# Performance work log

Measured on AMD Instinct MI355X. Metric: run time of the kernel, lower is better.

The kernel has to match this reference:

```python
import jax, jax.numpy as jnp
import numpy as np

B, S, H = 2, 1024, 4096
NH, NKV, HD = 32, 8, 128
THETA = 500000.0
EPS = 1e-6


def _ste(x, q):
    # straight-through estimator: forward q, gradient of identity
    return x + jax.lax.stop_gradient(q - x)


def weight_quant(w):
    # BitNet b1.58 ternary weight quantization (per-tensor mean-abs scale)
    scale = 1.0 / jnp.clip(jnp.mean(jnp.abs(w)), 1e-5)
    wq = jnp.clip(jnp.round(w * scale), -1.0, 1.0) / scale
    return _ste(w, wq)


def act_quant(x):
    # per-token int8 absmax activation quantization
    scale = 127.0 / jnp.clip(jnp.max(jnp.abs(x), axis=-1, keepdims=True), 1e-5)
    xq = jnp.clip(jnp.round(x * scale), -128.0, 127.0) / scale
    return _ste(x, xq)


def bitlinear(x, w):
    # torch Linear convention: w is (out, in)
    return act_quant(x) @ weight_quant(w).T


def rmsnorm(x, w):
    return x * jax.lax.rsqrt(jnp.mean(x * x, axis=-1, keepdims=True) + EPS) * w


def rope(x, cos, sin):
    # x: (b, s, h, hd); pairs are interleaved (even, odd) like view_as_complex
    x2 = x.reshape(*x.shape[:-1], HD // 2, 2)
    a, b = x2[..., 0], x2[..., 1]
    c = cos[None, :, None, :]
    s = sin[None, :, None, :]
    out = jnp.stack([a * c - b * s, a * s + b * c], axis=-1)
    return out.reshape(x.shape)


def setup_inputs() -> dict:
    key = jax.random.key(0)
    ks = jax.random.split(key, 6)
    hidden_states = jax.random.normal(ks[0], (B, S, H), dtype=jnp.float32)
    causal = jnp.tril(jnp.ones((S, S), dtype=bool))
    attention_mask = jnp.where(causal, 0.0, -1e9).astype(jnp.float32)[None, None]
    w_q = jax.random.normal(ks[1], (NH * HD, H), dtype=jnp.float32) * 0.02
    w_k = jax.random.normal(ks[2], (NKV * HD, H), dtype=jnp.float32) * 0.02
    w_v = jax.random.normal(ks[3], (NKV * HD, H), dtype=jnp.float32) * 0.02
    w_o = jax.random.normal(ks[4], (H, NH * HD), dtype=jnp.float32) * 0.02
    subln_w = jnp.ones((NH * HD,), dtype=jnp.float32)
    return {"hidden_states": hidden_states, "attention_mask": attention_mask,
            "w_q": w_q, "w_k": w_k, "w_v": w_v, "w_o": w_o, "subln_w": subln_w}


def reference(hidden_states, attention_mask, w_q, w_k, w_v, w_o, subln_w):
    b, s, _ = hidden_states.shape
    # RoPE tables (precomputed buffer in torch, constant here)
    inv_freq = 1.0 / (THETA ** (jnp.arange(0, HD, 2, dtype=jnp.float32) / HD))
    freqs = jnp.arange(s, dtype=jnp.float32)[:, None] * inv_freq[None, :]  # (s, hd/2)
    cos, sin = jnp.cos(freqs), jnp.sin(freqs)

    q = bitlinear(hidden_states, w_q).reshape(b, s, NH, HD)
    k = bitlinear(hidden_states, w_k).reshape(b, s, NKV, HD)
    v = bitlinear(hidden_states, w_v).reshape(b, s, NKV, HD)

    q = rope(q, cos, sin)
    k = rope(k, cos, sin)

    # GQA: repeat kv heads
    n_rep = NH // NKV
    k = jnp.repeat(k, n_rep, axis=2)  # (b, s, NH, hd)
    v = jnp.repeat(v, n_rep, axis=2)

    scale = 1.0 / np.sqrt(HD)
    scores = jnp.einsum('bqhd,bkhd->bhqk', q, k) * scale
    scores = scores + attention_mask
    attn = jax.nn.softmax(scores.astype(jnp.float32), axis=-1).astype(q.dtype)
    out = jnp.einsum('bhqk,bkhd->bqhd', attn, v).reshape(b, s, NH * HD)

    out = rmsnorm(out, subln_w)  # SubLN before output projection
    out = bitlinear(out, w_o)
    return out
```

## Files before the change

### kernel.cpp

```cpp
#include <hip/hip_runtime.h>
#include <hip/hip_bf16.h>
#include <cstdint>

typedef unsigned short u16;
typedef __bf16 bf16x8 __attribute__((ext_vector_type(8)));
typedef float f32x4 __attribute__((ext_vector_type(4)));
typedef int i32x4 __attribute__((ext_vector_type(4)));

#define SEQ 1024
#define HID 4096
#define NHQ 32
#define NKVH 8
#define HDIM 128
#define NB 2
#define NROWS (NB*SEQ)

static __device__ __forceinline__ u16 f2bf(float x) {
  __hip_bfloat16 h = __float2bfloat16(x);
  return *reinterpret_cast<u16*>(&h);
}

static __device__ __forceinline__ void gload16(const void* g, void* l) {
  __builtin_amdgcn_global_load_lds((__attribute__((address_space(1))) void*)(void*)g,
                                   (__attribute__((address_space(3))) void*)l, 16, 0, 0);
}

static __device__ __forceinline__ int pack4i8(float a, float b, float c, float d,
                                              float s, float lo, float hi) {
  int x0 = (int)fminf(fmaxf(rintf(a*s), lo), hi);
  int x1 = (int)fminf(fmaxf(rintf(b*s), lo), hi);
  int x2 = (int)fminf(fmaxf(rintf(c*s), lo), hi);
  int x3 = (int)fminf(fmaxf(rintf(d*s), lo), hi);
  return (x0 & 255) | ((x1 & 255) << 8) | ((x2 & 255) << 16) | ((x3 & 255) << 24);
}

__global__ __launch_bounds__(256) void k_abssum4(const float* __restrict__ wq_, const float* __restrict__ wk_,
                                                 const float* __restrict__ wv_, const float* __restrict__ wo_,
                                                 float* __restrict__ partial) {
  int bx = blockIdx.x;
  const float* w; long n4; int pbase, lb, nb;
  if (bx < 1024)      { w = wq_; n4 = 4194304; pbase = 0;    lb = bx;        nb = 1024; }
  else if (bx < 1280) { w = wk_; n4 = 1048576; pbase = 1024; lb = bx - 1024; nb = 256; }
  else if (bx < 1536) { w = wv_; n4 = 1048576; pbase = 1280; lb = bx - 1280; nb = 256; }
  else                { w = wo_; n4 = 4194304; pbase = 1536; lb = bx - 1536; nb = 1024; }
  float s = 0.f;
  long stride = (long)nb * 256;
  const float4* w4 = (const float4*)w;
  for (long j = (long)lb*256 + threadIdx.x; j < n4; j += stride) {
    float4 v = w4[j];
    s += fabsf(v.x) + fabsf(v.y) + fabsf(v.z) + fabsf(v.w);
  }
  #pragma unroll
  for (int off = 1; off < 64; off <<= 1) s += __shfl_xor(s, off);
  __shared__ float red[4];
  if ((threadIdx.x & 63) == 0) red[threadIdx.x >> 6] = s;
  __syncthreads();
  if (threadIdx.x == 0) partial[pbase + lb] = red[0] + red[1] + red[2] + red[3];
}

__global__ __launch_bounds__(256) void k_wscale(const float* __restrict__ partial,
                                                float* __restrict__ wsc) {
  __shared__ float red[4];
  const float nelem[4] = {16777216.f, 4194304.f, 4194304.f, 16777216.f};
  const int pbase[4] = {0, 1024, 1280, 1536};
  const int pcnt[4]  = {1024, 256, 256, 1024};
  for (int wi = 0; wi < 4; ++wi) {
    float s = 0.f;
    for (int j = threadIdx.x; j < pcnt[wi]; j += 256) s += partial[pbase[wi] + j];
    #pragma unroll
    for (int off = 1; off < 64; off <<= 1) s += __shfl_xor(s, off);
    if ((threadIdx.x & 63) == 0) red[threadIdx.x >> 6] = s;
    __syncthreads();
    if (threadIdx.x == 0) wsc[wi] = fmaxf((red[0]+red[1]+red[2]+red[3]) / nelem[wi], 1e-5f);
    __syncthreads();
  }
}

__global__ __launch_bounds__(256) void k_quantw8_all(const float* __restrict__ wq_, const float* __restrict__ wk_,
                                                     const float* __restrict__ wv_, const float* __restrict__ wo_,
                                                     char* __restrict__ oq_, char* __restrict__ ok_,
                                                     char* __restrict__ ov_, char* __restrict__ oo_,
                                                     const float* __restrict__ wsc) {
  int bx = blockIdx.x;
  const float* src; char* dst; int idx; long base;
  if (bx < 16384)      { src = wq_; dst = oq_; idx = 0; base = bx; }
  else if (bx < 20480) { src = wk_; dst = ok_; idx = 1; base = bx - 16384; }
  else if (bx < 24576) { src = wv_; dst = ov_; idx = 2; base = bx - 20480; }
  else                 { src = wo_; dst = oo_; idx = 3; base = bx - 24576; }
  long j = base*256 + threadIdx.x;
  long oj = j;
  if (idx <= 1) {
    long row = j >> 10;
    int u = (int)(row & 31);
    long prow = (row & ~31L) | (long)((u >> 1) | ((u & 1) << 4));
    oj = (prow << 10) | (j & 1023);
  }
  float inv = 1.0f / wsc[idx];
  float4 v = ((const float4*)src)[j];
  ((int*)dst)[oj] = pack4i8(v.x, v.y, v.z, v.w, inv, -1.f, 1.f);
}

__global__ __launch_bounds__(256) void k_actq8(const float* __restrict__ x, char* __restrict__ xq,
                                               float* __restrict__ xs) {
  long row = blockIdx.x;
  const float4* xr = (const float4*)(x + row*HID);
  float4 v[4];
  float am = 0.f;
  #pragma unroll
  for (int j = 0; j < 4; ++j) {
    v[j] = xr[j*256 + threadIdx.x];
    am = fmaxf(am, fmaxf(fmaxf(fabsf(v[j].x), fabsf(v[j].y)), fmaxf(fabsf(v[j].z), fabsf(v[j].w))));
  }
  #pragma unroll
  for (int off = 1; off < 64; off <<= 1) am = fmaxf(am, __shfl_xor(am, off));
  __shared__ float red[4];
  if ((threadIdx.x & 63) == 0) red[threadIdx.x >> 6] = am;
  __syncthreads();
  am = fmaxf(fmaxf(red[0], red[1]), fmaxf(red[2], red[3]));
  float amc = fmaxf(am, 1e-5f);
  float s = 127.0f / amc;
  int* oq = (int*)(xq + row*HID);
  #pragma unroll
  for (int j = 0; j < 4; ++j)
    oq[j*256 + threadIdx.x] = pack4i8(v[j].x, v[j].y, v[j].z, v[j].w, s, -128.f, 127.f);
  if (threadIdx.x == 0) xs[row] = amc / 127.0f;
}

__global__ __launch_bounds__(128, 2) void k_gemm8(const char* __restrict__ A, const char* __restrict__ W,
                                                  float* __restrict__ C, const float* __restrict__ arow,
                                                  const float* __restrict__ wsc, int widx,
                                                  int M, int N, int K) {
  __shared__ char As[3][128*64] __attribute__((aligned(16)));
  __shared__ char Ws_[3][128*64] __attribute__((aligned(16)));
  int t = threadIdx.x;
  int bid = blockIdx.x;
  int xcd = bid & 7, w = bid >> 3;
  int bm = ((xcd & 1) << 3) + (w >> 3);
  int bn = ((xcd >> 1) << 3) + (w & 7);
  const char* Ab = A + (long)bm*128*K;
  const char* Wb = W + (long)bn*128*K;
  int lane = t & 63, wid = t >> 6;
  int lrow = lane & 15, l8 = lane >> 4;
  int ch0 = (l8 ^ ((lrow >> 1) & 3)) * 16;
  i32x4 zero = {0, 0, 0, 0};
  i32x4 acc[4][8];
  #pragma unroll
  for (int mi = 0; mi < 4; ++mi)
    #pragma unroll
    for (int ni = 0; ni < 8; ++ni) acc[mi][ni] = zero;

  auto stage = [&](int buf, int kt) {
    #pragma unroll
    for (int i = 0; i < 4; ++i) {
      int c = t + 128*i;
      int row = c >> 2;
      int ci = ((c & 3) ^ ((row >> 1) & 3)) * 16;
      gload16(Ab + (long)row*K + kt*64 + ci, &As[buf][c*16]);
      gload16(Wb + (long)row*K + kt*64 + ci, &Ws_[buf][c*16]);
    }
  };

  int nk = K >> 6;
  stage(0, 0); stage(1, 1);
  asm volatile("s_waitcnt vmcnt(8)" ::: "memory");
  __builtin_amdgcn_sched_barrier(0);
  __builtin_amdgcn_s_barrier();
  __builtin_amdgcn_sched_barrier(0);
  for (int kt = 0; kt < nk; ++kt) {
    int cur = kt % 3;
    i32x4 af[4], bfr[8];
    #pragma unroll
    for (int mi = 0; mi < 4; ++mi) af[mi] = *(const i32x4*)&As[cur][(wid*64 + mi*16 + lrow)*64 + ch0];
    #pragma unroll
    for (int ni = 0; ni < 8; ++ni) bfr[ni] = *(const i32x4*)&Ws_[cur][(ni*16 + lrow)*64 + ch0];
    if (kt + 2 < nk) stage((kt + 2) % 3, kt + 2);
    __builtin_amdgcn_s_setprio(1);
    #pragma unroll
    for (int mi = 0; mi < 4; ++mi)
      #pragma unroll
      for (int ni = 0; ni < 8; ++ni)
        acc[mi][ni] = __builtin_amdgcn_mfma_i32_16x16x64_i8(af[mi], bfr[ni], acc[mi][ni], 0, 0, 0);
    __builtin_amdgcn_s_setprio(0);
    if (kt + 2 < nk)      asm volatile("s_waitcnt vmcnt(8)" ::: "memory");
    else if (kt + 1 < nk) asm volatile("s_waitcnt vmcnt(0)" ::: "memory");
    if (kt + 1 < nk) {
      __builtin_amdgcn_sched_barrier(0);
      __builtin_amdgcn_s_barrier();
      __builtin_amdgcn_sched_barrier(0);
    }
  }
  float ws = wsc[widx];
  #pragma unroll
  for (int mi = 0; mi < 4; ++mi)
    #pragma unroll
    for (int r = 0; r < 4; ++r) {
      int row = bm*128 + wid*64 + mi*16 + l8*4 + r;
      float sc = arow[row] * ws;
      #pragma unroll
      for (int ni = 0; ni < 8; ++ni) {
        int col = bn*128 + ni*16 + lrow;
        C[(long)row*N + col] = (float)acc[mi][ni][r] * sc;
      }
    }
}

__global__ __launch_bounds__(128, 2) void k_gemm8_qkv(const char* __restrict__ A,
    const char* __restrict__ Wq, const char* __restrict__ Wk, const char* __restrict__ Wv,
    u16* __restrict__ Qb, u16* __restrict__ Kb, u16* __restrict__ Vt,
    const float* __restrict__ arow, const float* __restrict__ wsc,
    const float* __restrict__ cosb, const float* __restrict__ sinb) {
  const int K = 4096;
  int bid = blockIdx.x;
  int xcd = bid & 7, w = bid >> 3;
  int kind, bm, bn;
  const char* W;
  if (w < 64)      { kind = 0; bm = ((xcd & 1) << 3) + (w >> 3); bn = ((xcd >> 1) << 3) + (w & 7); W = Wq; }
  else if (w < 80) { int u = w - 64; kind = 1; bm = (xcd << 1) + (u >> 3); bn = u & 7; W = Wk; }
  else             { int u = w - 80; kind = 2; bm = (xcd << 1) + (u >> 3); bn = u & 7; W = Wv; }

  __shared__ char As[3][128*64] __attribute__((aligned(16)));
  __shared__ char Ws_[3][128*64] __attribute__((aligned(16)));
  int t = threadIdx.x;
  const char* Ab = A + (long)bm*128*K;
  const char* Wb = W + (long)bn*128*K;
  int lane = t & 63, wid = t >> 6;
  int lrow = lane & 15, l8 = lane >> 4;
  int ch0 = (l8 ^ ((lrow >> 1) & 3)) * 16;
  i32x4 zero = {0, 0, 0, 0};
  i32x4 acc[4][8];
  #pragma unroll
  for (int mi = 0; mi < 4; ++mi)
    #pragma unroll
    for (int ni = 0; ni < 8; ++ni) acc[mi][ni] = zero;

  auto stage = [&](int buf, int kt) {
    #pragma unroll
    for (int i = 0; i < 4; ++i) {
      int c = t + 128*i;
      int row = c >> 2;
      int ci = ((c & 3) ^ ((row >> 1) & 3)) * 16;
      gload16(Ab + (long)row*K + kt*64 + ci, &As[buf][c*16]);
      gload16(Wb + (long)row*K + kt*64 + ci, &Ws_[buf][c*16]);
    }
  };

  int nk = K >> 6;
  stage(0, 0); stage(1, 1);
  asm volatile("s_waitcnt vmcnt(8)" ::: "memory");
  __builtin_amdgcn_sched_barrier(0);
  __builtin_amdgcn_s_barrier();
  __builtin_amdgcn_sched_barrier(0);
  for (int kt = 0; kt < nk; ++kt) {
    int cur = kt % 3;
    i32x4 af[4], bfr[8];
    #pragma unroll
    for (int mi = 0; mi < 4; ++mi) af[mi] = *(const i32x4*)&As[cur][(wid*64 + mi*16 + lrow)*64 + ch0];
    #pragma unroll
    for (int ni = 0; ni < 8; ++ni) bfr[ni] = *(const i32x4*)&Ws_[cur][(ni*16 + lrow)*64 + ch0];
    if (kt + 2 < nk) stage((kt + 2) % 3, kt + 2);
    __builtin_amdgcn_s_setprio(1);
    #pragma unroll
    for (int mi = 0; mi < 4; ++mi)
      #pragma unroll
      for (int ni = 0; ni < 8; ++ni)
        acc[mi][ni] = __builtin_amdgcn_mfma_i32_16x16x64_i8(af[mi], bfr[ni], acc[mi][ni], 0, 0, 0);
    __builtin_amdgcn_s_setprio(0);
    if (kt + 2 < nk)      asm volatile("s_waitcnt vmcnt(8)" ::: "memory");
    else if (kt + 1 < nk) asm volatile("s_waitcnt vmcnt(0)" ::: "memory");
    if (kt + 1 < nk) {
      __builtin_amdgcn_sched_barrier(0);
      __builtin_amdgcn_s_barrier();
      __builtin_amdgcn_sched_barrier(0);
    }
  }

  if (kind == 2) {
    float ws = wsc[2];
    #pragma unroll
    for (int mi = 0; mi < 4; ++mi) {
      int row0 = bm*128 + wid*64 + mi*16 + l8*4;
      int bidx = row0 >> 10, s0 = row0 & 1023;
      #pragma unroll
      for (int ni = 0; ni < 8; ++ni) {
        int col = bn*128 + ni*16 + lrow;
        int hkv = col >> 7, d = col & 127;
        ushort4 o4;
        o4.x = f2bf((float)acc[mi][ni][0] * arow[row0+0] * ws);
        o4.y = f2bf((float)acc[mi][ni][1] * arow[row0+1] * ws);
        o4.z = f2bf((float)acc[mi][ni][2] * arow[row0+2] * ws);
        o4.w = f2bf((float)acc[mi][ni][3] * arow[row0+3] * ws);
        *(ushort4*)&Vt[(((long)bidx*NKVH + hkv)*HDIM + d)*SEQ + s0] = o4;
      }
    }
  } else {
    float ws = wsc[kind];
    u16* dst = kind ? Kb : Qb;
    int nh = kind ? NKVH : NHQ;
    #pragma unroll
    for (int mi = 0; mi < 4; ++mi) {
      #pragma unroll
      for (int r = 0; r < 4; ++r) {
        int row = bm*128 + wid*64 + mi*16 + l8*4 + r;
        int bidx = row >> 10, s = row & 1023;
        float sc = arow[row] * ws;
        #pragma unroll
        for (int j = 0; j < 4; ++j) {
          float a  = (float)acc[mi][2*j][r] * sc;
          float b2 = (float)acc[mi][2*j+1][r] * sc;
          int B = bn*128 + j*32;
          int h = B >> 7;
          int d = (B & 127) + 2*lrow;
          int i = d >> 1;
          float cc = cosb[(s << 6) + i], sn = sinb[(s << 6) + i];
          ushort2 o2;
          o2.x = f2bf(a*cc - b2*sn);
          o2.y = f2bf(a*sn + b2*cc);
          *(ushort2*)&dst[(((long)bidx*nh + h)*SEQ + s)*HDIM + d] = o2;
        }
      }
    }
  }
}

__global__ __launch_bounds__(256) void k_ropetab(float* __restrict__ cosb, float* __restrict__ sinb) {
  int idx = blockIdx.x*256 + threadIdx.x;
  int s = idx >> 6, i = idx & 63;
  float e = (2.0f * (float)i) / 128.0f;
  float inv = 1.0f / powf(500000.0f, e);
  float f = (float)s * inv;
  cosb[idx] = cosf(f);
  sinb[idx] = sinf(f);
}

__global__ __launch_bounds__(256) void k_attn(const u16* __restrict__ qb, const u16* __restrict__ kb,
                                              const u16* __restrict__ vt, float* __restrict__ ao) {
  int p = blockIdx.x, h = blockIdx.y, b = blockIdx.z;
  int t = threadIdx.x, lane = t & 63, wid = t >> 6;
  int lrow = lane & 15, l8 = lane >> 4;
  int x7 = lrow & 7;

  __shared__ u16 Ks[2][64*128] __attribute__((aligned(16)));
  __shared__ u16 Vs[2][128*64] __attribute__((aligned(16)));
  __shared__ u16 Ps[4][16][72] __attribute__((aligned(16)));

  const u16* kp = kb + ((long)(b*NKVH + (h >> 2)))*SEQ*HDIM;
  const u16* vp = vt + ((long)(b*NKVH + (h >> 2)))*HDIM*SEQ;

  auto stageK = [&](int buf, int j) {
    const u16* src = kp + (long)j*64*HDIM;
    #pragma unroll
    for (int i = 0; i < 4; ++i) {
      int r0 = wid*16 + i*4;
      int row = r0 + (lane >> 4);
      int cg = (lane & 15) ^ (row & 7);
      gload16(src + (long)row*HDIM + cg*8, &Ks[buf][r0*HDIM]);
    }
  };
  auto stageV = [&](int buf, int j) {
    #pragma unroll
    for (int i = 0; i < 4; ++i) {
      int r0 = wid*32 + i*8;
      int row = r0 + (lane >> 3);
      int cg = (lane & 7) ^ (row & 7);
      gload16(vp + (long)row*SEQ + j*64 + cg*8, &Vs[buf][r0*64]);
    }
  };

  for (int phase = 0; phase < 2; ++phase) {
    int qt = phase ? (15 - p) : p;
    int q0 = qt*64 + wid*16;
    const u16* qp = qb + (((long)(b*NHQ + h))*SEQ + q0)*HDIM;
    bf16x8 qf[4];
    #pragma unroll
    for (int ks = 0; ks < 4; ++ks) qf[ks] = *(const bf16x8*)&qp[lrow*HDIM + ks*32 + l8*8];
    f32x4 zero = {0.f, 0.f, 0.f, 0.f};
    f32x4 o[8];
    #pragma unroll
    for (int f = 0; f < 8; ++f) o[f] = zero;
    float m[4], ll[4];
    #pragma unroll
    for (int r = 0; r < 4; ++r) { m[r] = -1e30f; ll[r] = 0.f; }

    int nj = qt + 1;
    stageK(0, 0); stageV(0, 0);
    __syncthreads();
    int cur = 0;
    for (int j = 0; j < nj; ++j) {
      if (j + 1 < nj) { stageK(cur ^ 1, j + 1); stageV(cur ^ 1, j + 1); }
      const u16* Kc = Ks[cur];
      const u16* Vc = Vs[cur];
      f32x4 sc4[4];
      #pragma unroll
      for (int ni = 0; ni < 4; ++ni) sc4[ni] = zero;
      __builtin_amdgcn_s_setprio(1);
      #pragma unroll
      for (int ni = 0; ni < 4; ++ni) {
        int row = ni*16 + lrow;
        #pragma unroll
        for (int ks = 0; ks < 4; ++ks) {
          int cl = (ks*4 + l8) ^ x7;
          bf16x8 kfr = *(const bf16x8*)&Kc[row*HDIM + cl*8];
          sc4[ni] = __builtin_amdgcn_mfma_f32_16x16x32_bf16(qf[ks], kfr, sc4[ni], 0, 0, 0);
        }
      }
      __builtin_amdgcn_s_setprio(0);
      const float scale = 0.08838834764831845f;
      float pm[4] = {-1e30f, -1e30f, -1e30f, -1e30f};
      float pv[4][4];
      bool diag = (j == qt);
      #pragma unroll
      for (int ni = 0; ni < 4; ++ni) {
        int kv = j*64 + ni*16 + lrow;
        #pragma unroll
        for (int r = 0; r < 4; ++r) {
          int qr = q0 + l8*4 + r;
          float val = sc4[ni][r] * scale;
          if (diag && kv > qr) val = -1e30f;
          pv[ni][r] = val;
          pm[r] = fmaxf(pm[r], val);
        }
      }
      #pragma unroll
      for (int r = 0; r < 4; ++r) {
        #pragma unroll
        for (int off = 1; off < 16; off <<= 1) pm[r] = fmaxf(pm[r], __shfl_xor(pm[r], off));
      }
      float fr[4], rs[4];
      #pragma unroll
      for (int r = 0; r < 4; ++r) {
        float nm = fmaxf(m[r], pm[r]);
        fr[r] = __expf(m[r] - nm);
        m[r] = nm; rs[r] = 0.f;
      }
      #pragma unroll
      for (int ni = 0; ni < 4; ++ni)
        #pragma unroll
        for (int r = 0; r < 4; ++r) {
          float pe = __expf(pv[ni][r] - m[r]);
          pv[ni][r] = pe; rs[r] += pe;
        }
      #pragma unroll
      for (int r = 0; r < 4; ++r) {
        #pragma unroll
        for (int off = 1; off < 16; off <<= 1) rs[r] += __shfl_xor(rs[r], off);
        ll[r] = ll[r]*fr[r] + rs[r];
      }
      #pragma unroll
      for (int f = 0; f < 8; ++f) {
        o[f][0] *= fr[0]; o[f][1] *= fr[1]; o[f][2] *= fr[2]; o[f][3] *= fr[3];
      }
      #pragma unroll
      for (int ni = 0; ni < 4; ++ni)
        #pragma unroll
        for (int r = 0; r < 4; ++r)
          Ps[wid][l8*4 + r][ni*16 + lrow] = f2bf(pv[ni][r]);
      bf16x8 pf0 = *(const bf16x8*)&Ps[wid][lrow][l8*8];
      bf16x8 pf1 = *(const bf16x8*)&Ps[wid][lrow][32 + l8*8];
      __builtin_amdgcn_s_setprio(1);
      #pragma unroll
      for (int f = 0; f < 8; ++f) {
        int d = f*16 + lrow;
        bf16x8 v0 = *(const bf16x8*)&Vc[d*64 + ((l8) ^ x7)*8];
        bf16x8 v1 = *(const bf16x8*)&Vc[d*64 + ((4 + l8) ^ x7)*8];
        o[f] = __builtin_amdgcn_mfma_f32_16x16x32_bf16(pf0, v0, o[f], 0, 0, 0);
        o[f] = __builtin_amdgcn_mfma_f32_16x16x32_bf16(pf1, v1, o[f], 0, 0, 0);
      }
      __builtin_amdgcn_s_setprio(0);
      __syncthreads();
      cur ^= 1;
    }
    float invl[4];
    #pragma unroll
    for (int r = 0; r < 4; ++r) invl[r] = 1.0f / ll[r];
    #pragma unroll
    for (int f = 0; f < 8; ++f)
      #pragma unroll
      for (int r = 0; r < 4; ++r) {
        long row = (long)b*SEQ + q0 + l8*4 + r;
        ao[row*HID + h*HDIM + f*16 + lrow] = o[f][r] * invl[r];
      }
    __syncthreads();
  }
}

__global__ __launch_bounds__(256) void k_rmsq8(const float* __restrict__ x, const float* __restrict__ w,
                                               char* __restrict__ yq, float* __restrict__ ys) {
  long row = blockIdx.x;
  const float4* xr = (const float4*)(x + row*HID);
  const float4* wr = (const float4*)w;
  float4 v[4];
  float ss = 0.f;
  #pragma unroll
  for (int j = 0; j < 4; ++j) {
    v[j] = xr[j*256 + threadIdx.x];
    ss += v[j].x*v[j].x + v[j].y*v[j].y + v[j].z*v[j].z + v[j].w*v[j].w;
  }
  #pragma unroll
  for (int off = 1; off < 64; off <<= 1) ss += __shfl_xor(ss, off);
  __shared__ float red[4];
  if ((threadIdx.x & 63) == 0) red[threadIdx.x >> 6] = ss;
  __syncthreads();
  ss = red[0] + red[1] + red[2] + red[3];
  __syncthreads();
  float rn = rsqrtf(ss / (float)HID + 1e-6f);
  float4 y[4];
  float am = 0.f;
  #pragma unroll
  for (int j = 0; j < 4; ++j) {
    float4 wv = wr[j*256 + threadIdx.x];
    y[j].x = v[j].x * rn * wv.x; y[j].y = v[j].y * rn * wv.y;
    y[j].z = v[j].z * rn * wv.z; y[j].w = v[j].w * rn * wv.w;
    am = fmaxf(am, fmaxf(fmaxf(fabsf(y[j].x), fabsf(y[j].y)), fmaxf(fabsf(y[j].z), fabsf(y[j].w))));
  }
  #pragma unroll
  for (int off = 1; off < 64; off <<= 1) am = fmaxf(am, __shfl_xor(am, off));
  if ((threadIdx.x & 63) == 0) red[threadIdx.x >> 6] = am;
  __syncthreads();
  am = fmaxf(fmaxf(red[0], red[1]), fmaxf(red[2], red[3]));
  float amc = fmaxf(am, 1e-5f);
  float s = 127.0f / amc;
  int* oq = (int*)(yq + row*HID);
  #pragma unroll
  for (int j = 0; j < 4; ++j)
    oq[j*256 + threadIdx.x] = pack4i8(y[j].x, y[j].y, y[j].z, y[j].w, s, -128.f, 127.f);
  if (threadIdx.x == 0) ys[row] = amc / 127.0f;
}

extern "C" void kernel_launch(void* const* d_in, const int* in_sizes, int n_in,
                              void* d_out, int out_size, void* d_ws, size_t ws_size,
                              hipStream_t stream) {
  const float* hs    = (const float*)d_in[0];
  const float* w_q   = (const float*)d_in[2];
  const float* w_k   = (const float*)d_in[3];
  const float* w_v   = (const float*)d_in[4];
  const float* w_o   = (const float*)d_in[5];
  const float* subln = (const float*)d_in[6];

  char* ws = (char*)d_ws;
  char*  wqq = (char*)(ws + 0L);
  char*  wqk = (char*)(ws + 16777216L);
  char*  wqv = (char*)(ws + 20971520L);
  char*  wqo = (char*)(ws + 25165824L);
  char*  xq  = (char*)(ws + 41943040L);
  float* ao  = (float*)(ws + 50331648L);
  char*  yq  = (char*)(ws + 83886080L);
  u16*   qb  = (u16*)(ws + 92274688L);
  u16*   kb  = (u16*)(ws + 109051904L);
  u16*   vtb = (u16*)(ws + 113246208L);
  float* cosb= (float*)(ws + 117440512L);
  float* sinb= (float*)(ws + 117702656L);
  float* xs  = (float*)(ws + 117964800L);
  float* ys  = (float*)(ws + 117972992L);
  float* wsc = (float*)(ws + 117981184L);
  float* par = (float*)(ws + 117981248L);
  float* out = (float*)d_out;

  k_abssum4<<<2560, 256, 0, stream>>>(w_q, w_k, w_v, w_o, par);
  k_wscale<<<1, 256, 0, stream>>>(par, wsc);

  k_quantw8_all<<<40960, 256, 0, stream>>>(w_q, w_k, w_v, w_o, wqq, wqk, wqv, wqo, wsc);
  k_ropetab<<<256, 256, 0, stream>>>(cosb, sinb);
  k_actq8<<<NROWS, 256, 0, stream>>>(hs, xq, xs);

  k_gemm8_qkv<<<768, 128, 0, stream>>>(xq, wqq, wqk, wqv, qb, kb, vtb, xs, wsc, cosb, sinb);

  k_attn<<<dim3(8, 32, 2), 256, 0, stream>>>(qb, kb, vtb, ao);

  k_rmsq8<<<NROWS, 256, 0, stream>>>(ao, subln, yq, ys);

  k_gemm8<<<512, 128, 0, stream>>>(yq, wqo, out, ys, wsc, 3, NROWS, 4096, 4096);
}
```

Before: 245.9 us.

## Load A operand directly into registers, bypassing LDS in int8 GEMMs

In both int8 GEMM kernels, each wave now loads its own A-operand rows straight from global memory into registers. A one-step register double buffer (afC/afN) holds the fragments, and the k-loop is unrolled by two so the buffers swap each step. A is no longer staged through LDS, and only W keeps the triple-buffered LDS path. This drops A's LDS writes and reads and halves shared memory use, since A rows are private to each wave. The explicit vmcnt waits are removed, so visibility of the LDS-DMA loads for W now depends on the compiler's in-order waits on the A register loads. The k-loop also now assumes an even tile count.

Result: slower. 278.3 us (+13.2%).

```diff
diff --git a/kernel.cpp b/kernel.cpp
--- a/kernel.cpp
+++ b/kernel.cpp
@@ -130,7 +130,6 @@
                                                   float* __restrict__ C, const float* __restrict__ arow,
                                                   const float* __restrict__ wsc, int widx,
                                                   int M, int N, int K) {
-  __shared__ char As[3][128*64] __attribute__((aligned(16)));
   __shared__ char Ws_[3][128*64] __attribute__((aligned(16)));
   int t = threadIdx.x;
   int bid = blockIdx.x;
@@ -142,6 +141,7 @@
   int lane = t & 63, wid = t >> 6;
   int lrow = lane & 15, l8 = lane >> 4;
   int ch0 = (l8 ^ ((lrow >> 1) & 3)) * 16;
+  const char* Aw = Ab + (long)(wid*64 + lrow)*K + l8*16;
   i32x4 zero = {0, 0, 0, 0};
   i32x4 acc[4][8];
   #pragma unroll
@@ -155,40 +155,49 @@
       int c = t + 128*i;
       int row = c >> 2;
       int ci = ((c & 3) ^ ((row >> 1) & 3)) * 16;
-      gload16(Ab + (long)row*K + kt*64 + ci, &As[buf][c*16]);
       gload16(Wb + (long)row*K + kt*64 + ci, &Ws_[buf][c*16]);
     }
   };
+  auto loadA = [&](i32x4* dst, int kt) {
+    #pragma unroll
+    for (int mi = 0; mi < 4; ++mi)
+      dst[mi] = *(const i32x4*)(Aw + (long)mi*16*K + kt*64);
+  };
 
   int nk = K >> 6;
+  i32x4 afC[4], afN[4];
   stage(0, 0); stage(1, 1);
+  loadA(afC, 0);
   asm volatile("s_waitcnt vmcnt(8)" ::: "memory");
   __builtin_amdgcn_sched_barrier(0);
   __builtin_amdgcn_s_barrier();
   __builtin_amdgcn_sched_barrier(0);
-  for (int kt = 0; kt < nk; ++kt) {
-    int cur = kt % 3;
-    i32x4 af[4], bfr[8];
-    #pragma unroll
-    for (int mi = 0; mi < 4; ++mi) af[mi] = *(const i32x4*)&As[cur][(wid*64 + mi*16 + lrow)*64 + ch0];
-    #pragma unroll
-    for (int ni = 0; ni < 8; ++ni) bfr[ni] = *(const i32x4*)&Ws_[cur][(ni*16 + lrow)*64 + ch0];
+
+  auto body = [&](int kt, i32x4* cur, i32x4* nxt) {
+    int cb = kt % 3;
+    i32x4 bfr[8];
+    #pragma unroll
+    for (int ni = 0; ni < 8; ++ni) bfr[ni] = *(const i32x4*)&Ws_[cb][(ni*16 + lrow)*64 + ch0];
     if (kt + 2 < nk) stage((kt + 2) % 3, kt + 2);
+    if (kt + 1 < nk) loadA(nxt, kt + 1);
     __builtin_amdgcn_s_setprio(1);
     #pragma unroll
     for (int mi = 0; mi < 4; ++mi)
       #pragma unroll
       for (int ni = 0; ni < 8; ++ni)
-        acc[mi][ni] = __builtin_amdgcn_mfma_i32_16x16x64_i8(af[mi], bfr[ni], acc[mi][ni], 0, 0, 0);
+        acc[mi][ni] = __builtin_amdgcn_mfma_i32_16x16x64_i8(cur[mi], bfr[ni], acc[mi][ni], 0, 0, 0);
     __builtin_amdgcn_s_setprio(0);
-    if (kt + 2 < nk)      asm volatile("s_waitcnt vmcnt(8)" ::: "memory");
-    else if (kt + 1 < nk) asm volatile("s_waitcnt vmcnt(0)" ::: "memory");
     if (kt + 1 < nk) {
       __builtin_amdgcn_sched_barrier(0);
       __builtin_amdgcn_s_barrier();
       __builtin_amdgcn_sched_barrier(0);
     }
-  }
+  };
+  for (int k2 = 0; k2 < nk; k2 += 2) {
+    body(k2, afC, afN);
+    body(k2 + 1, afN, afC);
+  }
+
   float ws = wsc[widx];
   #pragma unroll
   for (int mi = 0; mi < 4; ++mi)
@@ -218,7 +227,6 @@
   else if (w < 80) { int u = w - 64; kind = 1; bm = (xcd << 1) + (u >> 3); bn = u & 7; W = Wk; }
   else             { int u = w - 80; kind = 2; bm = (xcd << 1) + (u >> 3); bn = u & 7; W = Wv; }
 
-  __shared__ char As[3][128*64] __attribute__((aligned(16)));
   __shared__ char Ws_[3][128*64] __attribute__((aligned(16)));
   int t = threadIdx.x;
   const char* Ab = A + (long)bm*128*K;
@@ -226,6 +234,7 @@
   int lane = t & 63, wid = t >> 6;
   int lrow = lane & 15, l8 = lane >> 4;
   int ch0 = (l8 ^ ((lrow >> 1) & 3)) * 16;
+  const char* Aw = Ab + (long)(wid*64 + lrow)*K + l8*16;
   i32x4 zero = {0, 0, 0, 0};
   i32x4 acc[4][8];
   #pragma unroll
@@ -239,39 +248,47 @@
       int c = t + 128*i;
       int row = c >> 2;
       int ci = ((c & 3) ^ ((row >> 1) & 3)) * 16;
-      gload16(Ab + (long)row*K + kt*64 + ci, &As[buf][c*16]);
       gload16(Wb + (long)row*K + kt*64 + ci, &Ws_[buf][c*16]);
     }
   };
+  auto loadA = [&](i32x4* dst, int kt) {
+    #pragma unroll
+    for (int mi = 0; mi < 4; ++mi)
+      dst[mi] = *(const i32x4*)(Aw + (long)mi*16*K + kt*64);
+  };
 
   int nk = K >> 6;
+  i32x4 afC[4], afN[4];
   stage(0, 0); stage(1, 1);
+  loadA(afC, 0);
   asm volatile("s_waitcnt vmcnt(8)" ::: "memory");
   __builtin_amdgcn_sched_barrier(0);
   __builtin_amdgcn_s_barrier();
   __builtin_amdgcn_sched_barrier(0);
-  for (int kt = 0; kt < nk; ++kt) {
-    int cur = kt % 3;
-    i32x4 af[4], bfr[8];
-    #pragma unroll
-    for (int mi = 0; mi < 4; ++mi) af[mi] = *(const i32x4*)&As[cur][(wid*64 + mi*16 + lrow)*64 + ch0];
-    #pragma unroll
-    for (int ni = 0; ni < 8; ++ni) bfr[ni] = *(const i32x4*)&Ws_[cur][(ni*16 + lrow)*64 + ch0];
+
+  auto body = [&](int kt, i32x4* cur, i32x4* nxt) {
+    int cb = kt % 3;
+    i32x4 bfr[8];
+    #pragma unroll
+    for (int ni = 0; ni < 8; ++ni) bfr[ni] = *(const i32x4*)&Ws_[cb][(ni*16 + lrow)*64 + ch0];
     if (kt + 2 < nk) stage((kt + 2) % 3, kt + 2);
+    if (kt + 1 < nk) loadA(nxt, kt + 1);
     __builtin_amdgcn_s_setprio(1);
     #pragma unroll
     for (int mi = 0; mi < 4; ++mi)
       #pragma unroll
       for (int ni = 0; ni < 8; ++ni)
-        acc[mi][ni] = __builtin_amdgcn_mfma_i32_16x16x64_i8(af[mi], bfr[ni], acc[mi][ni], 0, 0, 0);
+        acc[mi][ni] = __builtin_amdgcn_mfma_i32_16x16x64_i8(cur[mi], bfr[ni], acc[mi][ni], 0, 0, 0);
     __builtin_amdgcn_s_setprio(0);
-    if (kt + 2 < nk)      asm volatile("s_waitcnt vmcnt(8)" ::: "memory");
-    else if (kt + 1 < nk) asm volatile("s_waitcnt vmcnt(0)" ::: "memory");
     if (kt + 1 < nk) {
       __builtin_amdgcn_sched_barrier(0);
       __builtin_amdgcn_s_barrier();
       __builtin_amdgcn_sched_barrier(0);
     }
+  };
+  for (int k2 = 0; k2 < nk; k2 += 2) {
+    body(k2, afC, afN);
+    body(k2 + 1, afN, afC);
   }
 
   if (kind == 2) {
```

## Merge preprocessing kernels and give attention waves two query tiles each

Applied to the files above, without the earlier changes.

The activation quantization is folded into the weight abs-sum kernel, and RoPE table generation is folded into the weight quantization kernel. Together these remove two kernel launches. The attention kernel now runs 2 waves per block, each handling 32 query rows (two 16-row MFMA tiles), so every K/V fragment read from LDS feeds two MFMAs. This halves the threads that stage the same K/V tiles, at the cost of higher register pressure and fewer waves in flight for latency hiding.

After: 274.8 us. 1.12x slower.

```diff
diff --git a/kernel.cpp b/kernel.cpp
--- a/kernel.cpp
+++ b/kernel.cpp
@@ -34,28 +34,54 @@
   return (x0 & 255) | ((x1 & 255) << 8) | ((x2 & 255) << 16) | ((x3 & 255) << 24);
 }
 
-__global__ __launch_bounds__(256) void k_abssum4(const float* __restrict__ wq_, const float* __restrict__ wk_,
-                                                 const float* __restrict__ wv_, const float* __restrict__ wo_,
-                                                 float* __restrict__ partial) {
+__global__ __launch_bounds__(256) void k_pass1(const float* __restrict__ wq_, const float* __restrict__ wk_,
+                                               const float* __restrict__ wv_, const float* __restrict__ wo_,
+                                               float* __restrict__ partial,
+                                               const float* __restrict__ x, char* __restrict__ xq,
+                                               float* __restrict__ xs) {
+  __shared__ float red[4];
   int bx = blockIdx.x;
-  const float* w; long n4; int pbase, lb, nb;
-  if (bx < 1024)      { w = wq_; n4 = 4194304; pbase = 0;    lb = bx;        nb = 1024; }
-  else if (bx < 1280) { w = wk_; n4 = 1048576; pbase = 1024; lb = bx - 1024; nb = 256; }
-  else if (bx < 1536) { w = wv_; n4 = 1048576; pbase = 1280; lb = bx - 1280; nb = 256; }
-  else                { w = wo_; n4 = 4194304; pbase = 1536; lb = bx - 1536; nb = 1024; }
-  float s = 0.f;
-  long stride = (long)nb * 256;
-  const float4* w4 = (const float4*)w;
-  for (long j = (long)lb*256 + threadIdx.x; j < n4; j += stride) {
-    float4 v = w4[j];
-    s += fabsf(v.x) + fabsf(v.y) + fabsf(v.z) + fabsf(v.w);
-  }
-  #pragma unroll
-  for (int off = 1; off < 64; off <<= 1) s += __shfl_xor(s, off);
-  __shared__ float red[4];
-  if ((threadIdx.x & 63) == 0) red[threadIdx.x >> 6] = s;
-  __syncthreads();
-  if (threadIdx.x == 0) partial[pbase + lb] = red[0] + red[1] + red[2] + red[3];
+  if (bx < 2560) {
+    const float* w; long n4; int pbase, lb, nb;
+    if (bx < 1024)      { w = wq_; n4 = 4194304; pbase = 0;    lb = bx;        nb = 1024; }
+    else if (bx < 1280) { w = wk_; n4 = 1048576; pbase = 1024; lb = bx - 1024; nb = 256; }
+    else if (bx < 1536) { w = wv_; n4 = 1048576; pbase = 1280; lb = bx - 1280; nb = 256; }
+    else                { w = wo_; n4 = 4194304; pbase = 1536; lb = bx - 1536; nb = 1024; }
+    float s = 0.f;
+    long stride = (long)nb * 256;
+    const float4* w4 = (const float4*)w;
+    for (long j = (long)lb*256 + threadIdx.x; j < n4; j += stride) {
+      float4 v = w4[j];
+      s += fabsf(v.x) + fabsf(v.y) + fabsf(v.z) + fabsf(v.w);
+    }
+    #pragma unroll
+    for (int off = 1; off < 64; off <<= 1) s += __shfl_xor(s, off);
+    if ((threadIdx.x & 63) == 0) red[threadIdx.x >> 6] = s;
+    __syncthreads();
+    if (threadIdx.x == 0) partial[pbase + lb] = red[0] + red[1] + red[2] + red[3];
+  } else {
+    long row = bx - 2560;
+    const float4* xr = (const float4*)(x + row*HID);
+    float4 v[4];
+    float am = 0.f;
+    #pragma unroll
+    for (int j = 0; j < 4; ++j) {
+      v[j] = xr[j*256 + threadIdx.x];
+      am = fmaxf(am, fmaxf(fmaxf(fabsf(v[j].x), fabsf(v[j].y)), fmaxf(fabsf(v[j].z), fabsf(v[j].w))));
+    }
+    #pragma unroll
+    for (int off = 1; off < 64; off <<= 1) am = fmaxf(am, __shfl_xor(am, off));
+    if ((threadIdx.x & 63) == 0) red[threadIdx.x >> 6] = am;
+    __syncthreads();
+    am = fmaxf(fmaxf(red[0], red[1]), fmaxf(red[2], red[3]));
+    float amc = fmaxf(am, 1e-5f);
+    float s = 127.0f / amc;
+    int* oq = (int*)(xq + row*HID);
+    #pragma unroll
+    for (int j = 0; j < 4; ++j)
+      oq[j*256 + threadIdx.x] = pack4i8(v[j].x, v[j].y, v[j].z, v[j].w, s, -128.f, 127.f);
+    if (threadIdx.x == 0) xs[row] = amc / 127.0f;
+  }
 }
 
 __global__ __launch_bounds__(256) void k_wscale(const float* __restrict__ partial,
@@ -80,8 +106,19 @@
                                                      const float* __restrict__ wv_, const float* __restrict__ wo_,
                                                      char* __restrict__ oq_, char* __restrict__ ok_,
                                                      char* __restrict__ ov_, char* __restrict__ oo_,
-                                                     const float* __restrict__ wsc) {
+                                                     const float* __restrict__ wsc,
+                                                     float* __restrict__ cosb, float* __restrict__ sinb) {
   int bx = blockIdx.x;
+  if (bx >= 40960) {
+    int idx = (bx - 40960)*256 + threadIdx.x;
+    int s = idx >> 6, i = idx & 63;
+    float e = (2.0f * (float)i) / 128.0f;
+    float inv = 1.0f / powf(500000.0f, e);
+    float f = (float)s * inv;
+    cosb[idx] = cosf(f);
+    sinb[idx] = sinf(f);
+    return;
+  }
   const float* src; char* dst; int idx; long base;
   if (bx < 16384)      { src = wq_; dst = oq_; idx = 0; base = bx; }
   else if (bx < 20480) { src = wk_; dst = ok_; idx = 1; base = bx - 16384; }
@@ -98,32 +135,6 @@
   float inv = 1.0f / wsc[idx];
   float4 v = ((const float4*)src)[j];
   ((int*)dst)[oj] = pack4i8(v.x, v.y, v.z, v.w, inv, -1.f, 1.f);
-}
-
-__global__ __launch_bounds__(256) void k_actq8(const float* __restrict__ x, char* __restrict__ xq,
-                                               float* __restrict__ xs) {
-  long row = blockIdx.x;
-  const float4* xr = (const float4*)(x + row*HID);
-  float4 v[4];
-  float am = 0.f;
-  #pragma unroll
-  for (int j = 0; j < 4; ++j) {
-    v[j] = xr[j*256 + threadIdx.x];
-    am = fmaxf(am, fmaxf(fmaxf(fabsf(v[j].x), fabsf(v[j].y)), fmaxf(fabsf(v[j].z), fabsf(v[j].w))));
-  }
-  #pragma unroll
-  for (int off = 1; off < 64; off <<= 1) am = fmaxf(am, __shfl_xor(am, off));
-  __shared__ float red[4];
-  if ((threadIdx.x & 63) == 0) red[threadIdx.x >> 6] = am;
-  __syncthreads();
-  am = fmaxf(fmaxf(red[0], red[1]), fmaxf(red[2], red[3]));
-  float amc = fmaxf(am, 1e-5f);
-  float s = 127.0f / amc;
-  int* oq = (int*)(xq + row*HID);
-  #pragma unroll
-  for (int j = 0; j < 4; ++j)
-    oq[j*256 + threadIdx.x] = pack4i8(v[j].x, v[j].y, v[j].z, v[j].w, s, -128.f, 127.f);
-  if (threadIdx.x == 0) xs[row] = amc / 127.0f;
 }
 
 __global__ __launch_bounds__(128, 2) void k_gemm8(const char* __restrict__ A, const char* __restrict__ W,
@@ -322,18 +333,8 @@
   }
 }
 
-__global__ __launch_bounds__(256) void k_ropetab(float* __restrict__ cosb, float* __restrict__ sinb) {
-  int idx = blockIdx.x*256 + threadIdx.x;
-  int s = idx >> 6, i = idx & 63;
-  float e = (2.0f * (float)i) / 128.0f;
-  float inv = 1.0f / powf(500000.0f, e);
-  float f = (float)s * inv;
-  cosb[idx] = cosf(f);
-  sinb[idx] = sinf(f);
-}
-
-__global__ __launch_bounds__(256) void k_attn(const u16* __restrict__ qb, const u16* __restrict__ kb,
-                                              const u16* __restrict__ vt, float* __restrict__ ao) {
+__global__ __launch_bounds__(128, 2) void k_attn(const u16* __restrict__ qb, const u16* __restrict__ kb,
+                                                 const u16* __restrict__ vt, float* __restrict__ ao) {
   int p = blockIdx.x, h = blockIdx.y, b = blockIdx.z;
   int t = threadIdx.x, lane = t & 63, wid = t >> 6;
   int lrow = lane & 15, l8 = lane >> 4;
@@ -341,7 +342,7 @@
 
   __shared__ u16 Ks[2][64*128] __attribute__((aligned(16)));
   __shared__ u16 Vs[2][128*64] __attribute__((aligned(16)));
-  __shared__ u16 Ps[4][16][72] __attribute__((aligned(16)));
+  __shared__ u16 Ps[2][32][72] __attribute__((aligned(16)));
 
   const u16* kp = kb + ((long)(b*NKVH + (h >> 2)))*SEQ*HDIM;
   const u16* vp = vt + ((long)(b*NKVH + (h >> 2)))*HDIM*SEQ;
@@ -349,8 +350,8 @@
   auto stageK = [&](int buf, int j) {
     const u16* src = kp + (long)j*64*HDIM;
     #pragma unroll
-    for (int i = 0; i < 4; ++i) {
-      int r0 = wid*16 + i*4;
+    for (int i = 0; i < 8; ++i) {
+      int r0 = wid*32 + i*4;
       int row = r0 + (lane >> 4);
       int cg = (lane & 15) ^ (row & 7);
       gload16(src + (long)row*HDIM + cg*8, &Ks[buf][r0*HDIM]);
@@ -358,8 +359,8 @@
   };
   auto stageV = [&](int buf, int j) {
     #pragma unroll
-    for (int i = 0; i < 4; ++i) {
-      int r0 = wid*32 + i*8;
+    for (int i = 0; i < 8; ++i) {
+      int r0 = wid*64 + i*8;
       int row = r0 + (lane >> 3);
       int cg = (lane & 7) ^ (row & 7);
       gload16(vp + (long)row*SEQ + j*64 + cg*8, &Vs[buf][r0*64]);
@@ -368,18 +369,25 @@
 
   for (int phase = 0; phase < 2; ++phase) {
     int qt = phase ? (15 - p) : p;
-    int q0 = qt*64 + wid*16;
+    int q0 = qt*64 + wid*32;
     const u16* qp = qb + (((long)(b*NHQ + h))*SEQ + q0)*HDIM;
-    bf16x8 qf[4];
-    #pragma unroll
-    for (int ks = 0; ks < 4; ++ks) qf[ks] = *(const bf16x8*)&qp[lrow*HDIM + ks*32 + l8*8];
+    bf16x8 qf[2][4];
+    #pragma unroll
+    for (int mi = 0; mi < 2; ++mi)
+      #pragma unroll
+      for (int ks = 0; ks < 4; ++ks)
+        qf[mi][ks] = *(const bf16x8*)&qp[(mi*16 + lrow)*HDIM + ks*32 + l8*8];
     f32x4 zero = {0.f, 0.f, 0.f, 0.f};
-    f32x4 o[8];
-    #pragma unroll
-    for (int f = 0; f < 8; ++f) o[f] = zero;
-    float m[4], ll[4];
-    #pragma unroll
-    for (int r = 0; r < 4; ++r) { m[r] = -1e30f; ll[r] = 0.f; }
+    f32x4 o[2][8];
+    #pragma unroll
+    for (int mi = 0; mi < 2; ++mi)
+      #pragma unroll
+      for (int f = 0; f < 8; ++f) o[mi][f] = zero;
+    float m[2][4], ll[2][4];
+    #pragma unroll
+    for (int mi = 0; mi < 2; ++mi)
+      #pragma unroll
+      for (int r = 0; r < 4; ++r) { m[mi][r] = -1e30f; ll[mi][r] = 0.f; }
 
     int nj = qt + 1;
     stageK(0, 0); stageV(0, 0);
@@ -389,9 +397,11 @@
       if (j + 1 < nj) { stageK(cur ^ 1, j + 1); stageV(cur ^ 1, j + 1); }
       const u16* Kc = Ks[cur];
       const u16* Vc = Vs[cur];
-      f32x4 sc4[4];
-      #pragma unroll
-      for (int ni = 0; ni < 4; ++ni) sc4[ni] = zero;
+      f32x4 sc4[2][4];
+      #pragma unroll
+      for (int mi = 0; mi < 2; ++mi)
+        #pragma unroll
+        for (int ni = 0; ni < 4; ++ni) sc4[mi][ni] = zero;
       __builtin_amdgcn_s_setprio(1);
       #pragma unroll
       for (int ni = 0; ni < 4; ++ni) {
@@ -400,85 +410,102 @@
         for (int ks = 0; ks < 4; ++ks) {
           int cl = (ks*4 + l8) ^ x7;
           bf16x8 kfr = *(const bf16x8*)&Kc[row*HDIM + cl*8];
-          sc4[ni] = __builtin_amdgcn_mfma_f32_16x16x32_bf16(qf[ks], kfr, sc4[ni], 0, 0, 0);
+          sc4[0][ni] = __builtin_amdgcn_mfma_f32_16x16x32_bf16(qf[0][ks], kfr, sc4[0][ni], 0, 0, 0);
+          sc4[1][ni] = __builtin_amdgcn_mfma_f32_16x16x32_bf16(qf[1][ks], kfr, sc4[1][ni], 0, 0, 0);
         }
       }
       __builtin_amdgcn_s_setprio(0);
       const float scale = 0.08838834764831845f;
-      float pm[4] = {-1e30f, -1e30f, -1e30f, -1e30f};
-      float pv[4][4];
+      float pm[2][4], pvv[2][4][4];
       bool diag = (j == qt);
       #pragma unroll
-      for (int ni = 0; ni < 4; ++ni) {
-        int kv = j*64 + ni*16 + lrow;
+      for (int mi = 0; mi < 2; ++mi) {
+        #pragma unroll
+        for (int r = 0; r < 4; ++r) pm[mi][r] = -1e30f;
+        #pragma unroll
+        for (int ni = 0; ni < 4; ++ni) {
+          int kv = j*64 + ni*16 + lrow;
+          #pragma unroll
+          for (int r = 0; r < 4; ++r) {
+            int qr = q0 + mi*16 + l8*4 + r;
+            float val = sc4[mi][ni][r] * scale;
+            if (diag && kv > qr) val = -1e30f;
+            pvv[mi][ni][r] = val;
+            pm[mi][r] = fmaxf(pm[mi][r], val);
+          }
+        }
+      }
+      float fr[2][4];
+      #pragma unroll
+      for (int mi = 0; mi < 2; ++mi) {
         #pragma unroll
         for (int r = 0; r < 4; ++r) {
-          int qr = q0 + l8*4 + r;
-          float val = sc4[ni][r] * scale;
-          if (diag && kv > qr) val = -1e30f;
-          pv[ni][r] = val;
-          pm[r] = fmaxf(pm[r], val);
-        }
-      }
-      #pragma unroll
-      for (int r = 0; r < 4; ++r) {
-        #pragma unroll
-        for (int off = 1; off < 16; off <<= 1) pm[r] = fmaxf(pm[r], __shfl_xor(pm[r], off));
-      }
-      float fr[4], rs[4];
-      #pragma unroll
-      for (int r = 0; r < 4; ++r) {
-        float nm = fmaxf(m[r], pm[r]);
-        fr[r] = __expf(m[r] - nm);
-        m[r] = nm; rs[r] = 0.f;
-      }
-      #pragma unroll
-      for (int ni = 0; ni < 4; ++ni)
+          #pragma unroll
+          for (int off = 1; off < 16; off <<= 1) pm[mi][r] = fmaxf(pm[mi][r], __shfl_xor(pm[mi][r], off));
+          float nm = fmaxf(m[mi][r], pm[mi][r]);
+          fr[mi][r] = __expf(m[mi][r] - nm);
+          m[mi][r] = nm;
+        }
+        float rs[4] = {0.f, 0.f, 0.f, 0.f};
+        #pragma unroll
+        for (int ni = 0; ni < 4; ++ni)
+          #pragma unroll
+          for (int r = 0; r < 4; ++r) {
+            float pe = __expf(pvv[mi][ni][r] - m[mi][r]);
+            pvv[mi][ni][r] = pe; rs[r] += pe;
+          }
         #pragma unroll
         for (int r = 0; r < 4; ++r) {
-          float pe = __expf(pv[ni][r] - m[r]);
-          pv[ni][r] = pe; rs[r] += pe;
-        }
-      #pragma unroll
-      for (int r = 0; r < 4; ++r) {
-        #pragma unroll
-        for (int off = 1; off < 16; off <<= 1) rs[r] += __shfl_xor(rs[r], off);
-        ll[r] = ll[r]*fr[r] + rs[r];
-      }
-      #pragma unroll
-      for (int f = 0; f < 8; ++f) {
-        o[f][0] *= fr[0]; o[f][1] *= fr[1]; o[f][2] *= fr[2]; o[f][3] *= fr[3];
-      }
-      #pragma unroll
-      for (int ni = 0; ni < 4; ++ni)
-        #pragma unroll
-        for (int r = 0; r < 4; ++r)
-          Ps[wid][l8*4 + r][ni*16 + lrow] = f2bf(pv[ni][r]);
-      bf16x8 pf0 = *(const bf16x8*)&Ps[wid][lrow][l8*8];
-      bf16x8 pf1 = *(const bf16x8*)&Ps[wid][lrow][32 + l8*8];
+          #pragma unroll
+          for (int off = 1; off < 16; off <<= 1) rs[r] += __shfl_xor(rs[r], off);
+          ll[mi][r] = ll[mi][r]*fr[mi][r] + rs[r];
+        }
+        #pragma unroll
+        for (int f = 0; f < 8; ++f) {
+          o[mi][f][0] *= fr[mi][0]; o[mi][f][1] *= fr[mi][1];
+          o[mi][f][2] *= fr[mi][2]; o[mi][f][3] *= fr[mi][3];
+        }
+        #pragma unroll
+        for (int ni = 0; ni < 4; ++ni)
+          #pragma unroll
+          for (int r = 0; r < 4; ++r)
+            Ps[wid][mi*16 + l8*4 + r][ni*16 + lrow] = f2bf(pvv[mi][ni][r]);
+      }
+      bf16x8 pf[2][2];
+      #pragma unroll
+      for (int mi = 0; mi < 2; ++mi) {
+        pf[mi][0] = *(const bf16x8*)&Ps[wid][mi*16 + lrow][l8*8];
+        pf[mi][1] = *(const bf16x8*)&Ps[wid][mi*16 + lrow][32 + l8*8];
+      }
       __builtin_amdgcn_s_setprio(1);
       #pragma unroll
       for (int f = 0; f < 8; ++f) {
         int d = f*16 + lrow;
         bf16x8 v0 = *(const bf16x8*)&Vc[d*64 + ((l8) ^ x7)*8];
         bf16x8 v1 = *(const bf16x8*)&Vc[d*64 + ((4 + l8) ^ x7)*8];
-        o[f] = __builtin_amdgcn_mfma_f32_16x16x32_bf16(pf0, v0, o[f], 0, 0, 0);
-        o[f] = __builtin_amdgcn_mfma_f32_16x16x32_bf16(pf1, v1, o[f], 0, 0, 0);
+        o[0][f] = __builtin_amdgcn_mfma_f32_16x16x32_bf16(pf[0][0], v0, o[0][f], 0, 0, 0);
+        o[0][f] = __builtin_amdgcn_mfma_f32_16x16x32_bf16(pf[0][1], v1, o[0][f], 0, 0, 0);
+        o[1][f] = __builtin_amdgcn_mfma_f32_16x16x32_bf16(pf[1][0], v0, o[1][f], 0, 0, 0);
+        o[1][f] = __builtin_amdgcn_mfma_f32_16x16x32_bf16(pf[1][1], v1, o[1][f], 0, 0, 0);
       }
       __builtin_amdgcn_s_setprio(0);
       __syncthreads();
       cur ^= 1;
     }
-    float invl[4];
-    #pragma unroll
-    for (int r = 0; r < 4; ++r) invl[r] = 1.0f / ll[r];
-    #pragma unroll
-    for (int f = 0; f < 8; ++f)
-      #pragma unroll
-      for (int r = 0; r < 4; ++r) {
-        long row = (long)b*SEQ + q0 + l8*4 + r;
-        ao[row*HID + h*HDIM + f*16 + lrow] = o[f][r] * invl[r];
-      }
+    float invl[2][4];
+    #pragma unroll
+    for (int mi = 0; mi < 2; ++mi)
+      #pragma unroll
+      for (int r = 0; r < 4; ++r) invl[mi][r] = 1.0f / ll[mi][r];
+    #pragma unroll
+    for (int mi = 0; mi < 2; ++mi)
+      #pragma unroll
+      for (int f = 0; f < 8; ++f)
+        #pragma unroll
+        for (int r = 0; r < 4; ++r) {
+          long row = (long)b*SEQ + q0 + mi*16 + l8*4 + r;
+          ao[row*HID + h*HDIM + f*16 + lrow] = o[mi][f][r] * invl[mi][r];
+        }
     __syncthreads();
   }
 }
@@ -555,16 +582,14 @@
   float* par = (float*)(ws + 117981248L);
   float* out = (float*)d_out;
 
-  k_abssum4<<<2560, 256, 0, stream>>>(w_q, w_k, w_v, w_o, par);
+  k_pass1<<<4608, 256, 0, stream>>>(w_q, w_k, w_v, w_o, par, hs, xq, xs);
   k_wscale<<<1, 256, 0, stream>>>(par, wsc);
 
-  k_quantw8_all<<<40960, 256, 0, stream>>>(w_q, w_k, w_v, w_o, wqq, wqk, wqv, wqo, wsc);
-  k_ropetab<<<256, 256, 0, stream>>>(cosb, sinb);
-  k_actq8<<<NROWS, 256, 0, stream>>>(hs, xq, xs);
+  k_quantw8_all<<<41216, 256, 0, stream>>>(w_q, w_k, w_v, w_o, wqq, wqk, wqv, wqo, wsc, cosb, sinb);
 
   k_gemm8_qkv<<<768, 128, 0, stream>>>(xq, wqq, wqk, wqv, qb, kb, vtb, xs, wsc, cosb, sinb);
 
-  k_attn<<<dim3(8, 32, 2), 256, 0, stream>>>(qb, kb, vtb, ao);
+  k_attn<<<dim3(8, 32, 2), 128, 0, stream>>>(qb, kb, vtb, ao);
 
   k_rmsq8<<<NROWS, 256, 0, stream>>>(ao, subln, yq, ys);
 
```
